# Performance work log

Measured on AMD Instinct MI355X. Metric: run time of the kernel, lower is better.

The kernel has to match this reference:

```python
import jax, jax.numpy as jnp
import numpy as np

EPS = 1e-12
ETA = 1.0


def _l2norm(x, eps=EPS):
    # torch F.normalize: x / max(||x||, eps)
    n = jnp.sqrt(jnp.sum(x * x, axis=-1, keepdims=True))
    return x / jnp.maximum(n, eps)


def setup_inputs() -> dict:
    key = jax.random.key(0)
    ks = jax.random.split(key, 7)
    B, IN, H = 256, 512, 512
    std = 1.0 / np.sqrt(H)
    return {
        "inputs": jax.random.normal(ks[0], (B, IN), jnp.float32),
        "hidden": jax.random.normal(ks[1], (B, H), jnp.float32),
        "assoc_mem": jax.random.normal(ks[2], (B, H, H), jnp.float32),
        "W_ih": jax.random.uniform(ks[3], (3 * H, IN), jnp.float32, -std, std),
        "b_ih": jax.random.uniform(ks[4], (3 * H,), jnp.float32, -std, std),
        "W_hh": jax.random.uniform(ks[5], (3 * H, H), jnp.float32, -std, std),
        "b_hh": jax.random.uniform(ks[6], (3 * H,), jnp.float32, -std, std),
    }


def reference(inputs, hidden, assoc_mem, W_ih, b_ih, W_hh, b_hh):
    H = hidden.shape[-1]
    # projections = ih(inputs) + hh(hidden)  -> [B, 3H]
    proj = inputs @ W_ih.T + b_ih + hidden @ W_hh.T + b_hh
    u_gate, r, x_emb = jnp.split(proj, 3, axis=1)

    # rotation_operator(x_emb, r): Householder-style rotation in span{u, v}
    u = _l2norm(x_emb)                                    # [B, H]
    r_n = _l2norm(r)
    costh = jnp.sum(u * r_n, axis=-1, keepdims=True)      # [B, 1]
    sinth = jnp.sqrt(1.0 - costh ** 2)                    # [B, 1]
    v = _l2norm(r - jnp.sum(u * r, axis=-1, keepdims=True) * u)

    # R = I - uu^T - vv^T + tmp^T Rth tmp
    #   = I + (cos-1)(uu^T + vv^T) + sin (v u^T - u v^T)
    uu = jnp.einsum('bi,bj->bij', u, u)
    vv = jnp.einsum('bi,bj->bij', v, v)
    cross = jnp.einsum('bi,bj->bij', v, u) - jnp.einsum('bi,bj->bij', u, v)
    R = (jnp.eye(H, dtype=hidden.dtype)
         + (costh - 1.0)[..., None] * (uu + vv)
         + sinth[..., None] * cross)                      # [B, H, H]

    # Rth = assoc_mem @ R ; hidden_new = Rth @ hidden
    Rth_full = jnp.einsum('bij,bjk->bik', assoc_mem, R)
    hidden_new = jnp.einsum('bij,bj->bi', Rth_full, hidden)

    c = jax.nn.relu(hidden_new + x_emb)
    new_h = u_gate * hidden + (1.0 - u_gate) * c
    new_h = _l2norm(new_h) * ETA
    return new_h
```

## Files before the change

kernel.cpp:

```cpp
#include <hip/hip_runtime.h>


#define EPSF 1e-12f

typedef float vfloat4 __attribute__((ext_vector_type(4)));

__global__ __launch_bounds__(256) void gemm_proj(
    const float* __restrict__ inp, const float* __restrict__ hid,
    const float* __restrict__ W_ih, const float* __restrict__ W_hh,
    const float* __restrict__ b_ih, const float* __restrict__ b_hh,
    float* __restrict__ proj)
{
    __shared__ float Xs[32 * 34];
    __shared__ float Ws[32 * 64];
    const int t  = threadIdx.x;
    const int tx = t & 15;
    const int ty = t >> 4;
    const int col0 = blockIdx.x * 64;
    const int row0 = blockIdx.y * 32;
    const int lr = t >> 3;
    const int lk = (t & 7) * 4;

    float acc[2][4] = {};

    float4 xv  = *(const float4*)(inp  + (size_t)(row0 + lr) * 512 + lk);
    float4 wv0 = *(const float4*)(W_ih + (size_t)(col0 + lr) * 512 + lk);
    float4 wv1 = *(const float4*)(W_ih + (size_t)(col0 + lr + 32) * 512 + lk);

    for (int cc = 0; cc < 32; ++cc) {
        __syncthreads();
        Xs[(lk + 0) * 34 + lr] = xv.x;
        Xs[(lk + 1) * 34 + lr] = xv.y;
        Xs[(lk + 2) * 34 + lr] = xv.z;
        Xs[(lk + 3) * 34 + lr] = xv.w;
        Ws[(lk + 0) * 64 + lr] = wv0.x;
        Ws[(lk + 1) * 64 + lr] = wv0.y;
        Ws[(lk + 2) * 64 + lr] = wv0.z;
        Ws[(lk + 3) * 64 + lr] = wv0.w;
        Ws[(lk + 0) * 64 + lr + 32] = wv1.x;
        Ws[(lk + 1) * 64 + lr + 32] = wv1.y;
        Ws[(lk + 2) * 64 + lr + 32] = wv1.z;
        Ws[(lk + 3) * 64 + lr + 32] = wv1.w;

        const int nc = (cc < 31) ? cc + 1 : 31;
        const float* Xg = (nc & 16) ? hid  : inp;
        const float* Wg = (nc & 16) ? W_hh : W_ih;
        const int k0 = (nc & 15) * 32;
        xv  = *(const float4*)(Xg + (size_t)(row0 + lr) * 512 + k0 + lk);
        wv0 = *(const float4*)(Wg + (size_t)(col0 + lr) * 512 + k0 + lk);
        wv1 = *(const float4*)(Wg + (size_t)(col0 + lr + 32) * 512 + k0 + lk);

        __syncthreads();
#pragma unroll
        for (int kk = 0; kk < 32; ++kk) {
            float2 xv2 = *(const float2*)&Xs[kk * 34 + 2 * ty];
            float4 wv4 = *(const float4*)&Ws[kk * 64 + 4 * tx];
            acc[0][0] += xv2.x * wv4.x;
            acc[0][1] += xv2.x * wv4.y;
            acc[0][2] += xv2.x * wv4.z;
            acc[0][3] += xv2.x * wv4.w;
            acc[1][0] += xv2.y * wv4.x;
            acc[1][1] += xv2.y * wv4.y;
            acc[1][2] += xv2.y * wv4.z;
            acc[1][3] += xv2.y * wv4.w;
        }
    }

    const float4 bi = *(const float4*)(b_ih + col0 + 4 * tx);
    const float4 bh = *(const float4*)(b_hh + col0 + 4 * tx);
    const float4 bias = { bi.x + bh.x, bi.y + bh.y, bi.z + bh.z, bi.w + bh.w };
#pragma unroll
    for (int i = 0; i < 2; ++i) {
        const int r = row0 + 2 * ty + i;
        float4 o = { acc[i][0] + bias.x, acc[i][1] + bias.y,
                     acc[i][2] + bias.z, acc[i][3] + bias.w };
        *(float4*)(proj + (size_t)r * 1536 + col0 + 4 * tx) = o;
    }
}


__device__ __forceinline__ float4 block_reduce4_1024(float4 v, float4* red, int t) {
    __syncthreads();
#pragma unroll
    for (int off = 32; off >= 1; off >>= 1) {
        v.x += __shfl_xor(v.x, off, 64);
        v.y += __shfl_xor(v.y, off, 64);
        v.z += __shfl_xor(v.z, off, 64);
        v.w += __shfl_xor(v.w, off, 64);
    }
    if ((t & 63) == 0) red[t >> 6] = v;
    __syncthreads();
    float4 s = {0.f, 0.f, 0.f, 0.f};
#pragma unroll
    for (int i = 0; i < 16; ++i) {
        float4 r = red[i];
        s.x += r.x; s.y += r.y; s.z += r.z; s.w += r.w;
    }
    return s;
}

__global__ __launch_bounds__(1024) void rum_fused(
    const float* __restrict__ proj, const float* __restrict__ hid,
    const float* __restrict__ A, float* __restrict__ out)
{
    __shared__ float4 Rh4[128];
    __shared__ float  hn[512];
    __shared__ float4 red[16];
    float* Rh = (float*)Rh4;

    const int b = blockIdx.x;
    const int t = threadIdx.x;
    const float* prow = proj + (size_t)b * 1536;

    float xe = 0.f, rr = 0.f, hh = 0.f;
    if (t < 512) {
        xe = prow[1024 + t];
        rr = prow[512 + t];
        hh = hid[(size_t)b * 512 + t];
    }
    float4 p1 = { xe * xe, rr * rr, xe * rr, xe * hh };
    p1 = block_reduce4_1024(p1, red, t);
    const float nx = fmaxf(sqrtf(p1.x), EPSF);
    const float nr = fmaxf(sqrtf(p1.y), EPSF);
    const float costh = p1.z / (nx * nr);
    const float sinth = sqrtf(fmaxf(1.0f - costh * costh, 0.0f));
    const float dot_ur = p1.z / nx;
    const float a = p1.w / nx;
    const float u = xe / nx;
    const float w = rr - dot_ur * u;

    float4 p2 = { w * w, w * hh, 0.f, 0.f };
    p2 = block_reduce4_1024(p2, red, t);
    const float nw = fmaxf(sqrtf(p2.x), EPSF);
    const float bb = p2.y / nw;
    const float v = w / nw;
    const float cm1 = costh - 1.0f;
    if (t < 512)
        Rh[t] = hh + cm1 * (a * u + bb * v) + sinth * (a * v - bb * u);
    __syncthreads();

    const int lane = t & 63;
    const int wv = t >> 6;
    const int g = lane >> 4;
    const int c = lane & 15;

    float4 xr[8];
#pragma unroll
    for (int k = 0; k < 8; ++k) xr[k] = Rh4[c + 16 * k];

    const vfloat4* Ab = (const vfloat4*)(A + (size_t)b * 512 * 512);
#pragma unroll 2
    for (int q = 0; q < 8; ++q) {
        const int i = 32 * wv + 4 * q + g;
        const vfloat4* Ar = Ab + (size_t)i * 128;
        float a0 = 0.f, a1 = 0.f, a2 = 0.f, a3 = 0.f;
#pragma unroll
        for (int k = 0; k < 8; k += 4) {
            vfloat4 v0 = __builtin_nontemporal_load(Ar + c + 16 * (k + 0));
            vfloat4 v1 = __builtin_nontemporal_load(Ar + c + 16 * (k + 1));
            vfloat4 v2 = __builtin_nontemporal_load(Ar + c + 16 * (k + 2));
            vfloat4 v3 = __builtin_nontemporal_load(Ar + c + 16 * (k + 3));
            a0 += v0.x * xr[k + 0].x + v0.y * xr[k + 0].y + v0.z * xr[k + 0].z + v0.w * xr[k + 0].w;
            a1 += v1.x * xr[k + 1].x + v1.y * xr[k + 1].y + v1.z * xr[k + 1].z + v1.w * xr[k + 1].w;
            a2 += v2.x * xr[k + 2].x + v2.y * xr[k + 2].y + v2.z * xr[k + 2].z + v2.w * xr[k + 2].w;
            a3 += v3.x * xr[k + 3].x + v3.y * xr[k + 3].y + v3.z * xr[k + 3].z + v3.w * xr[k + 3].w;
        }
        float accq = (a0 + a1) + (a2 + a3);
#pragma unroll
        for (int off = 8; off >= 1; off >>= 1)
            accq += __shfl_xor(accq, off, 16);
        if (c == 0) hn[i] = accq;
    }
    __syncthreads();

    float tv = 0.f, ug = 0.f;
    if (t < 512) {
        ug = prow[t];
        const float cx = fmaxf(hn[t] + xe, 0.0f);
        tv = ug * hh + (1.0f - ug) * cx;
    }
    float4 p3 = { tv * tv, 0.f, 0.f, 0.f };
    p3 = block_reduce4_1024(p3, red, t);
    const float inv = 1.0f / fmaxf(sqrtf(p3.x), EPSF);
    if (t < 512)
        out[(size_t)b * 512 + t] = tv * inv;
}

extern "C" void kernel_launch(void* const* d_in, const int* in_sizes, int n_in,
                              void* d_out, int out_size, void* d_ws, size_t ws_size,
                              hipStream_t stream)
{
    const float* inp  = (const float*)d_in[0];
    const float* hid  = (const float*)d_in[1];
    const float* A    = (const float*)d_in[2];
    const float* W_ih = (const float*)d_in[3];
    const float* b_ih = (const float*)d_in[4];
    const float* W_hh = (const float*)d_in[5];
    const float* b_hh = (const float*)d_in[6];
    float* out = (float*)d_out;

    float* proj = (float*)d_ws;

    gemm_proj<<<dim3(24, 8), 256, 0, stream>>>(inp, hid, W_ih, W_hh, b_ih, b_hh, proj);
    rum_fused<<<dim3(256), 1024, 0, stream>>>(proj, hid, A, out);
}
```

Measured before the change: 385.2 us.

## Retile projection GEMM, merge reductions, and prefetch assoc_mem rows early

The projection GEMM moves to 48-column tiles with K=64 chunks, double-buffered shared memory and a single barrier per step, and runs on 256 blocks to fill more CUs. The fused kernel issues its first row of assoc_mem loads before the norm reductions so memory latency overlaps with them. The second block reduction is removed by expressing ||w||² and w·h algebraically from the first-pass sums, and the final reduction is simplified to a scalar. Computing the norm of w this way may lose some floating-point accuracy through cancellation.

```diff
diff --git a/kernel.cpp b/kernel.cpp
--- a/kernel.cpp
+++ b/kernel.cpp
@@ -4,6 +4,8 @@
 #define EPSF 1e-12f
 
 typedef float vfloat4 __attribute__((ext_vector_type(4)));
+
+#define WSTR 49
 
 __global__ __launch_bounds__(256) void gemm_proj(
     const float* __restrict__ inp, const float* __restrict__ hid,
@@ -11,92 +13,93 @@
     const float* __restrict__ b_ih, const float* __restrict__ b_hh,
     float* __restrict__ proj)
 {
-    __shared__ float Xs[32 * 34];
-    __shared__ float Ws[32 * 64];
+    __shared__ float Xs[2][64 * 34];
+    __shared__ float Ws[2][64 * WSTR];
     const int t  = threadIdx.x;
     const int tx = t & 15;
     const int ty = t >> 4;
-    const int col0 = blockIdx.x * 64;
+    const int col0 = blockIdx.x * 48;
     const int row0 = blockIdx.y * 32;
     const int lr = t >> 3;
     const int lk = (t & 7) * 4;
-
-    float acc[2][4] = {};
-
-    float4 xv  = *(const float4*)(inp  + (size_t)(row0 + lr) * 512 + lk);
-    float4 wv0 = *(const float4*)(W_ih + (size_t)(col0 + lr) * 512 + lk);
-    float4 wv1 = *(const float4*)(W_ih + (size_t)(col0 + lr + 32) * 512 + lk);
-
-    for (int cc = 0; cc < 32; ++cc) {
+    const int wr = (t >> 4) * 3;
+    const int wk = (t & 15) * 4;
+
+    float acc[2][3] = {};
+
+    const float* Xg = inp;
+    const float* Wg = W_ih;
+    float4 xv0 = *(const float4*)(Xg + (size_t)(row0 + lr) * 512 + lk);
+    float4 xv1 = *(const float4*)(Xg + (size_t)(row0 + lr) * 512 + lk + 32);
+    float4 wv0 = *(const float4*)(Wg + (size_t)(col0 + wr + 0) * 512 + wk);
+    float4 wv1 = *(const float4*)(Wg + (size_t)(col0 + wr + 1) * 512 + wk);
+    float4 wv2 = *(const float4*)(Wg + (size_t)(col0 + wr + 2) * 512 + wk);
+
+    for (int cc = 0; cc < 16; ++cc) {
+        float* Xb = Xs[cc & 1];
+        float* Wb = Ws[cc & 1];
+        Xb[(lk + 0) * 34 + lr] = xv0.x;
+        Xb[(lk + 1) * 34 + lr] = xv0.y;
+        Xb[(lk + 2) * 34 + lr] = xv0.z;
+        Xb[(lk + 3) * 34 + lr] = xv0.w;
+        Xb[(lk + 32) * 34 + lr] = xv1.x;
+        Xb[(lk + 33) * 34 + lr] = xv1.y;
+        Xb[(lk + 34) * 34 + lr] = xv1.z;
+        Xb[(lk + 35) * 34 + lr] = xv1.w;
+        Wb[(wk + 0) * WSTR + wr + 0] = wv0.x;
+        Wb[(wk + 1) * WSTR + wr + 0] = wv0.y;
+        Wb[(wk + 2) * WSTR + wr + 0] = wv0.z;
+        Wb[(wk + 3) * WSTR + wr + 0] = wv0.w;
+        Wb[(wk + 0) * WSTR + wr + 1] = wv1.x;
+        Wb[(wk + 1) * WSTR + wr + 1] = wv1.y;
+        Wb[(wk + 2) * WSTR + wr + 1] = wv1.z;
+        Wb[(wk + 3) * WSTR + wr + 1] = wv1.w;
+        Wb[(wk + 0) * WSTR + wr + 2] = wv2.x;
+        Wb[(wk + 1) * WSTR + wr + 2] = wv2.y;
+        Wb[(wk + 2) * WSTR + wr + 2] = wv2.z;
+        Wb[(wk + 3) * WSTR + wr + 2] = wv2.w;
+
+        if (cc < 15) {
+            const int nc = cc + 1;
+            Xg = (nc & 8) ? hid  : inp;
+            Wg = (nc & 8) ? W_hh : W_ih;
+            const int k0 = (nc & 7) * 64;
+            xv0 = *(const float4*)(Xg + (size_t)(row0 + lr) * 512 + k0 + lk);
+            xv1 = *(const float4*)(Xg + (size_t)(row0 + lr) * 512 + k0 + lk + 32);
+            wv0 = *(const float4*)(Wg + (size_t)(col0 + wr + 0) * 512 + k0 + wk);
+            wv1 = *(const float4*)(Wg + (size_t)(col0 + wr + 1) * 512 + k0 + wk);
+            wv2 = *(const float4*)(Wg + (size_t)(col0 + wr + 2) * 512 + k0 + wk);
+        }
+
         __syncthreads();
-        Xs[(lk + 0) * 34 + lr] = xv.x;
-        Xs[(lk + 1) * 34 + lr] = xv.y;
-        Xs[(lk + 2) * 34 + lr] = xv.z;
-        Xs[(lk + 3) * 34 + lr] = xv.w;
-        Ws[(lk + 0) * 64 + lr] = wv0.x;
-        Ws[(lk + 1) * 64 + lr] = wv0.y;
-        Ws[(lk + 2) * 64 + lr] = wv0.z;
-        Ws[(lk + 3) * 64 + lr] = wv0.w;
-        Ws[(lk + 0) * 64 + lr + 32] = wv1.x;
-        Ws[(lk + 1) * 64 + lr + 32] = wv1.y;
-        Ws[(lk + 2) * 64 + lr + 32] = wv1.z;
-        Ws[(lk + 3) * 64 + lr + 32] = wv1.w;
-
-        const int nc = (cc < 31) ? cc + 1 : 31;
-        const float* Xg = (nc & 16) ? hid  : inp;
-        const float* Wg = (nc & 16) ? W_hh : W_ih;
-        const int k0 = (nc & 15) * 32;
-        xv  = *(const float4*)(Xg + (size_t)(row0 + lr) * 512 + k0 + lk);
-        wv0 = *(const float4*)(Wg + (size_t)(col0 + lr) * 512 + k0 + lk);
-        wv1 = *(const float4*)(Wg + (size_t)(col0 + lr + 32) * 512 + k0 + lk);
-
-        __syncthreads();
-#pragma unroll
-        for (int kk = 0; kk < 32; ++kk) {
-            float2 xv2 = *(const float2*)&Xs[kk * 34 + 2 * ty];
-            float4 wv4 = *(const float4*)&Ws[kk * 64 + 4 * tx];
-            acc[0][0] += xv2.x * wv4.x;
-            acc[0][1] += xv2.x * wv4.y;
-            acc[0][2] += xv2.x * wv4.z;
-            acc[0][3] += xv2.x * wv4.w;
-            acc[1][0] += xv2.y * wv4.x;
-            acc[1][1] += xv2.y * wv4.y;
-            acc[1][2] += xv2.y * wv4.z;
-            acc[1][3] += xv2.y * wv4.w;
+#pragma unroll 16
+        for (int kk = 0; kk < 64; ++kk) {
+            const float2 x2 = *(const float2*)&Xb[kk * 34 + 2 * ty];
+            const float w0 = Wb[kk * WSTR + 3 * tx + 0];
+            const float w1 = Wb[kk * WSTR + 3 * tx + 1];
+            const float w2 = Wb[kk * WSTR + 3 * tx + 2];
+            acc[0][0] += x2.x * w0; acc[0][1] += x2.x * w1; acc[0][2] += x2.x * w2;
+            acc[1][0] += x2.y * w0; acc[1][1] += x2.y * w1; acc[1][2] += x2.y * w2;
         }
     }
 
-    const float4 bi = *(const float4*)(b_ih + col0 + 4 * tx);
-    const float4 bh = *(const float4*)(b_hh + col0 + 4 * tx);
-    const float4 bias = { bi.x + bh.x, bi.y + bh.y, bi.z + bh.z, bi.w + bh.w };
+    const int cbase = col0 + 3 * tx;
+    const float bias0 = b_ih[cbase + 0] + b_hh[cbase + 0];
+    const float bias1 = b_ih[cbase + 1] + b_hh[cbase + 1];
+    const float bias2 = b_ih[cbase + 2] + b_hh[cbase + 2];
 #pragma unroll
     for (int i = 0; i < 2; ++i) {
         const int r = row0 + 2 * ty + i;
-        float4 o = { acc[i][0] + bias.x, acc[i][1] + bias.y,
-                     acc[i][2] + bias.z, acc[i][3] + bias.w };
-        *(float4*)(proj + (size_t)r * 1536 + col0 + 4 * tx) = o;
-    }
-}
-
-
-__device__ __forceinline__ float4 block_reduce4_1024(float4 v, float4* red, int t) {
-    __syncthreads();
-#pragma unroll
-    for (int off = 32; off >= 1; off >>= 1) {
-        v.x += __shfl_xor(v.x, off, 64);
-        v.y += __shfl_xor(v.y, off, 64);
-        v.z += __shfl_xor(v.z, off, 64);
-        v.w += __shfl_xor(v.w, off, 64);
-    }
-    if ((t & 63) == 0) red[t >> 6] = v;
-    __syncthreads();
-    float4 s = {0.f, 0.f, 0.f, 0.f};
-#pragma unroll
-    for (int i = 0; i < 16; ++i) {
-        float4 r = red[i];
-        s.x += r.x; s.y += r.y; s.z += r.z; s.w += r.w;
-    }
-    return s;
+        float* p = proj + (size_t)r * 1536 + cbase;
+        p[0] = acc[i][0] + bias0;
+        p[1] = acc[i][1] + bias1;
+        p[2] = acc[i][2] + bias2;
+    }
+}
+
+
+__device__ __forceinline__ float dot4(vfloat4 a, float4 b) {
+    return a.x * b.x + a.y * b.y + a.z * b.z + a.w * b.w;
 }
 
 __global__ __launch_bounds__(1024) void rum_fused(
@@ -106,51 +109,88 @@
     __shared__ float4 Rh4[128];
     __shared__ float  hn[512];
     __shared__ float4 red[16];
+    __shared__ float  red1[16];
     float* Rh = (float*)Rh4;
 
     const int b = blockIdx.x;
     const int t = threadIdx.x;
+    const int lane = t & 63;
+    const int wv = t >> 6;
+    const int g = lane >> 4;
+    const int c = lane & 15;
     const float* prow = proj + (size_t)b * 1536;
-
-    float xe = 0.f, rr = 0.f, hh = 0.f;
+    const vfloat4* Ab = (const vfloat4*)(A + (size_t)b * 262144);
+
+    const vfloat4* Ar0 = Ab + (size_t)(32 * wv + g) * 128;
+    vfloat4 pf[8];
+#pragma unroll
+    for (int k = 0; k < 8; ++k) pf[k] = __builtin_nontemporal_load(Ar0 + c + 16 * k);
+
+    float xe = 0.f, rr = 0.f, hh = 0.f, ug = 0.f;
     if (t < 512) {
         xe = prow[1024 + t];
         rr = prow[512 + t];
         hh = hid[(size_t)b * 512 + t];
-    }
-    float4 p1 = { xe * xe, rr * rr, xe * rr, xe * hh };
-    p1 = block_reduce4_1024(p1, red, t);
-    const float nx = fmaxf(sqrtf(p1.x), EPSF);
-    const float nr = fmaxf(sqrtf(p1.y), EPSF);
-    const float costh = p1.z / (nx * nr);
+        ug = prow[t];
+    }
+    float4 p = { xe * xe, rr * rr, xe * rr, xe * hh };
+    float pe = rr * hh;
+#pragma unroll
+    for (int off = 32; off >= 1; off >>= 1) {
+        p.x += __shfl_xor(p.x, off, 64);
+        p.y += __shfl_xor(p.y, off, 64);
+        p.z += __shfl_xor(p.z, off, 64);
+        p.w += __shfl_xor(p.w, off, 64);
+        pe  += __shfl_xor(pe,  off, 64);
+    }
+    if (lane == 0) { red[wv] = p; red1[wv] = pe; }
+    __syncthreads();
+    float xx = 0.f, r2 = 0.f, xr = 0.f, xh = 0.f, rh = 0.f;
+#pragma unroll
+    for (int i = 0; i < 16; ++i) {
+        float4 q = red[i];
+        xx += q.x; r2 += q.y; xr += q.z; xh += q.w; rh += red1[i];
+    }
+    const float nx = fmaxf(sqrtf(xx), EPSF);
+    const float nr = fmaxf(sqrtf(r2), EPSF);
+    const float costh = xr / (nx * nr);
     const float sinth = sqrtf(fmaxf(1.0f - costh * costh, 0.0f));
-    const float dot_ur = p1.z / nx;
-    const float a = p1.w / nx;
-    const float u = xe / nx;
-    const float w = rr - dot_ur * u;
-
-    float4 p2 = { w * w, w * hh, 0.f, 0.f };
-    p2 = block_reduce4_1024(p2, red, t);
-    const float nw = fmaxf(sqrtf(p2.x), EPSF);
-    const float bb = p2.y / nw;
-    const float v = w / nw;
+    const float inx2 = 1.0f / (nx * nx);
+    const float dot_ur = xr / nx;
+    const float a = xh / nx;
+    const float uu = xx * inx2;
+    const float ww = fmaxf(r2 - xr * xr * inx2 * (2.0f - uu), 0.0f);
+    const float wh = rh - xr * xh * inx2;
+    const float nw = fmaxf(sqrtf(ww), EPSF);
+    const float bb = wh / nw;
+    const float inw = 1.0f / nw;
     const float cm1 = costh - 1.0f;
-    if (t < 512)
+    if (t < 512) {
+        const float u = xe / nx;
+        const float w = rr - dot_ur * u;
+        const float v = w * inw;
         Rh[t] = hh + cm1 * (a * u + bb * v) + sinth * (a * v - bb * u);
-    __syncthreads();
-
-    const int lane = t & 63;
-    const int wv = t >> 6;
-    const int g = lane >> 4;
-    const int c = lane & 15;
-
-    float4 xr[8];
-#pragma unroll
-    for (int k = 0; k < 8; ++k) xr[k] = Rh4[c + 16 * k];
-
-    const vfloat4* Ab = (const vfloat4*)(A + (size_t)b * 512 * 512);
+    }
+    __syncthreads();
+
+    float4 xr4[8];
+#pragma unroll
+    for (int k = 0; k < 8; ++k) xr4[k] = Rh4[c + 16 * k];
+
+    {
+        const int i = 32 * wv + g;
+        float a0 = dot4(pf[0], xr4[0]) + dot4(pf[4], xr4[4]);
+        float a1 = dot4(pf[1], xr4[1]) + dot4(pf[5], xr4[5]);
+        float a2 = dot4(pf[2], xr4[2]) + dot4(pf[6], xr4[6]);
+        float a3 = dot4(pf[3], xr4[3]) + dot4(pf[7], xr4[7]);
+        float accq = (a0 + a1) + (a2 + a3);
+#pragma unroll
+        for (int off = 8; off >= 1; off >>= 1)
+            accq += __shfl_xor(accq, off, 16);
+        if (c == 0) hn[i] = accq;
+    }
 #pragma unroll 2
-    for (int q = 0; q < 8; ++q) {
+    for (int q = 1; q < 8; ++q) {
         const int i = 32 * wv + 4 * q + g;
         const vfloat4* Ar = Ab + (size_t)i * 128;
         float a0 = 0.f, a1 = 0.f, a2 = 0.f, a3 = 0.f;
@@ -160,10 +200,10 @@
             vfloat4 v1 = __builtin_nontemporal_load(Ar + c + 16 * (k + 1));
             vfloat4 v2 = __builtin_nontemporal_load(Ar + c + 16 * (k + 2));
             vfloat4 v3 = __builtin_nontemporal_load(Ar + c + 16 * (k + 3));
-            a0 += v0.x * xr[k + 0].x + v0.y * xr[k + 0].y + v0.z * xr[k + 0].z + v0.w * xr[k + 0].w;
-            a1 += v1.x * xr[k + 1].x + v1.y * xr[k + 1].y + v1.z * xr[k + 1].z + v1.w * xr[k + 1].w;
-            a2 += v2.x * xr[k + 2].x + v2.y * xr[k + 2].y + v2.z * xr[k + 2].z + v2.w * xr[k + 2].w;
-            a3 += v3.x * xr[k + 3].x + v3.y * xr[k + 3].y + v3.z * xr[k + 3].z + v3.w * xr[k + 3].w;
+            a0 += dot4(v0, xr4[k + 0]);
+            a1 += dot4(v1, xr4[k + 1]);
+            a2 += dot4(v2, xr4[k + 2]);
+            a3 += dot4(v3, xr4[k + 3]);
         }
         float accq = (a0 + a1) + (a2 + a3);
 #pragma unroll
@@ -173,15 +213,20 @@
     }
     __syncthreads();
 
-    float tv = 0.f, ug = 0.f;
+    float tv = 0.f;
     if (t < 512) {
-        ug = prow[t];
         const float cx = fmaxf(hn[t] + xe, 0.0f);
         tv = ug * hh + (1.0f - ug) * cx;
     }
-    float4 p3 = { tv * tv, 0.f, 0.f, 0.f };
-    p3 = block_reduce4_1024(p3, red, t);
-    const float inv = 1.0f / fmaxf(sqrtf(p3.x), EPSF);
+    float s = tv * tv;
+#pragma unroll
+    for (int off = 32; off >= 1; off >>= 1) s += __shfl_xor(s, off, 64);
+    if (lane == 0) red1[wv] = s;
+    __syncthreads();
+    float tot = 0.f;
+#pragma unroll
+    for (int i = 0; i < 16; ++i) tot += red1[i];
+    const float inv = 1.0f / fmaxf(sqrtf(tot), EPSF);
     if (t < 512)
         out[(size_t)b * 512 + t] = tv * inv;
 }
@@ -201,6 +246,6 @@
 
     float* proj = (float*)d_ws;
 
-    gemm_proj<<<dim3(24, 8), 256, 0, stream>>>(inp, hid, W_ih, W_hh, b_ih, b_hh, proj);
+    gemm_proj<<<dim3(32, 8), 256, 0, stream>>>(inp, hid, W_ih, W_hh, b_ih, b_hh, proj);
     rum_fused<<<dim3(256), 1024, 0, stream>>>(proj, hid, A, out);
 }
```

After: 388.4 us. About the same (+0.8%).
